# Kernel tuning notes

Measured on AMD Instinct MI355X. Metric: run time of the kernel, lower is better.

## Reference

```python
import jax, jax.numpy as jnp
import numpy as np

# PillarFeatureNet defaults
VX, VY = 0.2, 0.2
X_OFF = VX / 2 + 0.0      # vx/2 + pc_range[0]
Y_OFF = VY / 2 + (-40.0)  # vy/2 + pc_range[1]
BN_EPS = 1e-3             # mmdet3d BN1d eps for PFNLayer

P, N, C_RAW, C_OUT = 60000, 32, 4, 64  # pillars, max points/pillar, raw feats, PFN width


def setup_inputs() -> dict:
    key = jax.random.key(0)
    kf, kn, kc, kw = jax.random.split(key, 4)
    features = jax.random.normal(kf, (P, N, C_RAW), dtype=jnp.float32)
    # at least 1 valid point per pillar (original divides by num_points)
    num_points = jax.random.randint(kn, (P,), 1, N + 1, dtype=jnp.int32)
    coors = jax.random.randint(kc, (P, 4), 0, 352, dtype=jnp.int32)  # (batch, z, y, x) indices
    W = jax.random.normal(kw, (9, C_OUT), dtype=jnp.float32) * 0.1   # Linear(9,64,bias=False)
    gamma = jnp.ones((C_OUT,), jnp.float32)   # BN affine
    beta = jnp.zeros((C_OUT,), jnp.float32)
    return {"features": features, "num_points": num_points, "coors": coors,
            "W": W, "gamma": gamma, "beta": beta}


def reference(features, num_points, coors, W, gamma, beta):
    dt = features.dtype
    npts = num_points.astype(dt)[:, None, None]                    # [P,1,1]
    # cluster-center offset (xyz minus per-pillar mean over valid count)
    points_mean = jnp.sum(features[:, :, :3], axis=1, keepdims=True) / npts
    f_cluster = features[:, :, :3] - points_mean                   # [P,N,3]
    # voxel-center offset (xy minus pillar center from coors)
    xc = coors[:, 3].astype(dt)[:, None] * VX + X_OFF              # [P,1]
    yc = coors[:, 2].astype(dt)[:, None] * VY + Y_OFF
    f_center = jnp.stack([features[:, :, 0] - xc,
                          features[:, :, 1] - yc], axis=-1)        # [P,N,2]
    feats = jnp.concatenate([features, f_cluster, f_center], axis=-1)  # [P,N,9]
    # zero out padded points
    mask = (jnp.arange(feats.shape[1])[None, :] < num_points[:, None]).astype(dt)
    feats = feats * mask[:, :, None]
    # PFNLayer: Linear(no bias) -> BatchNorm1d (train-mode batch stats over P*N) -> ReLU -> max over points
    x = feats @ W                                                  # [P,N,64]
    mean = jnp.mean(x, axis=(0, 1))
    var = jnp.mean(jnp.square(x - mean), axis=(0, 1))              # biased, as torch BN training
    x = (x - mean) * (gamma / jnp.sqrt(var + BN_EPS)) + beta
    x = jax.nn.relu(x)
    return jnp.max(x, axis=1)                                      # [P,64] (squeeze(1) of keepdim max)
```

## Files before the change

### kernel.cpp

```cpp
#include <hip/hip_runtime.h>

#define NPT 32
#define COUT 64

typedef __fp16 v2hf __attribute__((ext_vector_type(2)));
typedef _Float16 v8h __attribute__((ext_vector_type(8)));
typedef float v16f __attribute__((ext_vector_type(16)));

union PKU { v2hf h; unsigned u; };
union FrgU { unsigned u[4]; v8h h; };

__device__ __forceinline__ unsigned pk2(float a, float b) {
    PKU p; p.h = __builtin_amdgcn_cvt_pkrtz(a, b); return p.u;
}

__device__ __forceinline__ float max16(v16f c) {
    float a = fmaxf(fmaxf(c[0], c[1]), fmaxf(c[2], c[3]));
    float b = fmaxf(fmaxf(c[4], c[5]), fmaxf(c[6], c[7]));
    float d = fmaxf(fmaxf(c[8], c[9]), fmaxf(c[10], c[11]));
    float e = fmaxf(fmaxf(c[12], c[13]), fmaxf(c[14], c[15]));
    return fmaxf(fmaxf(a, b), fmaxf(d, e));
}
__device__ __forceinline__ float sum16(v16f c) {
    float a = (c[0] + c[1]) + (c[2] + c[3]);
    float b = (c[4] + c[5]) + (c[6] + c[7]);
    float d = (c[8] + c[9]) + (c[10] + c[11]);
    float e = (c[12] + c[13]) + (c[14] + c[15]);
    return (a + b) + (d + e);
}
__device__ __forceinline__ float sumsq16(v16f c) {
    float a = 0.f, b = 0.f, d = 0.f, e = 0.f;
    #pragma unroll
    for (int i = 0; i < 4; i++) {
        a = fmaf(c[i], c[i], a);
        b = fmaf(c[4 + i], c[4 + i], b);
        d = fmaf(c[8 + i], c[8 + i], d);
        e = fmaf(c[12 + i], c[12 + i], e);
    }
    return (a + b) + (d + e);
}

__global__ __launch_bounds__(256, 3) void pillar_kernel(
        const float4* __restrict__ feat,
        const int* __restrict__ num_points,
        const int* __restrict__ coors,
        const float* __restrict__ W,
        float* __restrict__ out,
        float* __restrict__ stats,
        int P)
{
    __shared__ float red[4][128];

    int t = threadIdx.x;
    int lane = t & 63;
    int wv = t >> 6;
    int n = lane & 31;
    int hi = lane >> 5;
    int numPairs = (P + 1) >> 1;
    int pair = blockIdx.x * 4 + wv;

    float w4a = W[4 * COUT + n],      w5a = W[5 * COUT + n];
    float w6a = W[6 * COUT + n],      w7a = W[7 * COUT + n];
    float w8a = W[8 * COUT + n];
    float w4b = W[4 * COUT + 32 + n], w5b = W[5 * COUT + 32 + n];
    float w6b = W[6 * COUT + 32 + n], w7b = W[7 * COUT + 32 + n];
    float w8b = W[8 * COUT + 32 + n];
    float wp0a = W[0 * COUT + n] + w4a + w7a;
    float wp1a = W[1 * COUT + n] + w5a + w8a;
    float wp2a = W[2 * COUT + n] + w6a;
    float wp3a = W[3 * COUT + n];
    float wp0b = W[0 * COUT + 32 + n] + w4b + w7b;
    float wp1b = W[1 * COUT + 32 + n] + w5b + w8b;
    float wp2b = W[2 * COUT + 32 + n] + w6b;
    float wp3b = W[3 * COUT + 32 + n];
    unsigned bu0 = hi ? 0u : pk2(wp0a, wp1a);
    unsigned bu1 = hi ? 0u : pk2(wp2a, wp3a);
    unsigned bv0 = hi ? 0u : pk2(wp0b, wp1b);
    unsigned bv1 = hi ? 0u : pk2(wp2b, wp3b);

    int p = pair * 2 + hi;
    bool inb = (p < P);
    float4 f = make_float4(0.f, 0.f, 0.f, 0.f);
    int np = 1; float xc = 0.f, yc = 0.f;
    if (inb) {
        f  = feat[p * NPT + n];
        np = num_points[p];
        int2 cxy = *(const int2*)&coors[p * 4 + 2];
        yc = (float)cxy.x * 0.2f - 39.9f;
        xc = (float)cxy.y * 0.2f + 0.1f;
    }
    float sx = f.x, sy = f.y, sz = f.z;
    #pragma unroll
    for (int m = 1; m < 32; m <<= 1) {
        sx += __shfl_xor(sx, m);
        sy += __shfl_xor(sy, m);
        sz += __shfl_xor(sz, m);
    }
    float invn = 1.0f / (float)np;
    float mx = sx * invn, my = sy * invn, mz = sz * invn;
    float dA = mx * w4a + my * w5a + mz * w6a + xc * w7a + yc * w8a;
    float dB = mx * w4b + my * w5b + mz * w6b + xc * w7b + yc * w8b;
    float dA1 = __shfl_xor(dA, 32);
    float dB1 = __shfl_xor(dB, 32);

    bool msk = inb && (n < np);
    unsigned u0 = msk ? pk2(f.x, f.y) : 0u;
    unsigned u1 = msk ? pk2(f.z, f.w) : 0u;
    unsigned u2 = msk ? 0x3C00u : 0u;
    unsigned e0 = (unsigned)__shfl_xor((int)u0, 32);
    unsigned e1 = (unsigned)__shfl_xor((int)u1, 32);
    unsigned e2 = (unsigned)__shfl_xor((int)u2, 32);

    FrgU a0, a1;
    a0.u[0] = hi ? 0u : u0;  a0.u[1] = hi ? 0u : u1;
    a0.u[2] = hi ? 0u : u2;  a0.u[3] = 0u;
    a1.u[0] = hi ? 0u : e0;  a1.u[1] = hi ? 0u : e1;
    a1.u[2] = hi ? 0u : e2;  a1.u[3] = 0u;

    FrgU b00, b01, b10, b11;
    b00.u[0] = bu0; b00.u[1] = bu1; b00.u[2] = hi ? 0u : pk2(-dA,  0.f); b00.u[3] = 0u;
    b01.u[0] = bv0; b01.u[1] = bv1; b01.u[2] = hi ? 0u : pk2(-dB,  0.f); b01.u[3] = 0u;
    b10.u[0] = bu0; b10.u[1] = bu1; b10.u[2] = hi ? 0u : pk2(-dA1, 0.f); b10.u[3] = 0u;
    b11.u[0] = bv0; b11.u[1] = bv1; b11.u[2] = hi ? 0u : pk2(-dB1, 0.f); b11.u[3] = 0u;

    v16f cz = {};
    v16f c00 = __builtin_amdgcn_mfma_f32_32x32x16_f16(a0.h, b00.h, cz, 0, 0, 0);
    v16f c01 = __builtin_amdgcn_mfma_f32_32x32x16_f16(a0.h, b01.h, cz, 0, 0, 0);
    v16f c10 = __builtin_amdgcn_mfma_f32_32x32x16_f16(a1.h, b10.h, cz, 0, 0, 0);
    v16f c11 = __builtin_amdgcn_mfma_f32_32x32x16_f16(a1.h, b11.h, cz, 0, 0, 0);

    float s1a = sum16(c00) + sum16(c10);
    float s2a = sumsq16(c00) + sumsq16(c10);
    float s1b = sum16(c01) + sum16(c11);
    float s2b = sumsq16(c01) + sumsq16(c11);

    float m00 = max16(c00), m01 = max16(c01), m10 = max16(c10), m11 = max16(c11);
    m00 = fmaxf(m00, __shfl_xor(m00, 32));
    m01 = fmaxf(m01, __shfl_xor(m01, 32));
    m10 = fmaxf(m10, __shfl_xor(m10, 32));
    m11 = fmaxf(m11, __shfl_xor(m11, 32));

    int p0 = pair * 2;
    if (p0 < P)     out[p0 * COUT + lane]       = hi ? m01 : m00;
    if (p0 + 1 < P) out[(p0 + 1) * COUT + lane] = hi ? m11 : m10;

    s1a += __shfl_xor(s1a, 32);  s2a += __shfl_xor(s2a, 32);
    s1b += __shfl_xor(s1b, 32);  s2b += __shfl_xor(s2b, 32);
    red[wv][lane]      = hi ? s1b : s1a;
    red[wv][64 + lane] = hi ? s2b : s2a;
    __syncthreads();
    if (t < 128) {
        float s = red[0][t] + red[1][t] + red[2][t] + red[3][t];
        atomicAdd(&stats[(blockIdx.x & 7) * 128 + t], s);
    }
}

__global__ __launch_bounds__(256) void finalize_kernel(
        float4* __restrict__ out,
        const float* __restrict__ stats,
        const float* __restrict__ gamma,
        const float* __restrict__ beta,
        int n4, float invM)
{
    __shared__ float ss[128];
    int t = threadIdx.x;
    if (t < 64) {
        float s1 = 0.f, s2 = 0.f;
        #pragma unroll
        for (int x = 0; x < 8; x++) {
            s1 += stats[x * 128 + t];
            s2 += stats[x * 128 + 64 + t];
        }
        float mean = s1 * invM;
        float var = s2 * invM - mean * mean;
        float scale = gamma[t] * rsqrtf(var + 1e-3f);
        ss[t] = scale;
        ss[64 + t] = beta[t] - mean * scale;
    }
    __syncthreads();
    int i = blockIdx.x * 256 + t;
    if (i >= n4) return;
    int cb = (i & 15) * 4;
    float4 v = out[i];
    const float4 sc = *(const float4*)&ss[cb];
    const float4 sh = *(const float4*)&ss[64 + cb];
    v.x = fmaxf(fmaf(v.x, sc.x, sh.x), 0.f);
    v.y = fmaxf(fmaf(v.y, sc.y, sh.y), 0.f);
    v.z = fmaxf(fmaf(v.z, sc.z, sh.z), 0.f);
    v.w = fmaxf(fmaf(v.w, sc.w, sh.w), 0.f);
    out[i] = v;
}

extern "C" void kernel_launch(void* const* d_in, const int* in_sizes, int n_in,
                              void* d_out, int out_size, void* d_ws, size_t ws_size,
                              hipStream_t stream) {
    const float* features   = (const float*)d_in[0];
    const int*   num_points = (const int*)d_in[1];
    const int*   coors      = (const int*)d_in[2];
    const float* W          = (const float*)d_in[3];
    const float* gamma      = (const float*)d_in[4];
    const float* beta       = (const float*)d_in[5];
    float* out = (float*)d_out;
    int P = in_sizes[1];

    float* stats = (float*)d_ws;

    hipMemsetAsync(d_ws, 0, 8 * 128 * sizeof(float), stream);

    int numPairs = (P + 1) >> 1;
    int blocks1 = (numPairs + 3) / 4;
    pillar_kernel<<<blocks1, 256, 0, stream>>>((const float4*)features,
                                               num_points, coors, W, out,
                                               stats, P);
    int n4 = P * (COUT / 4);
    finalize_kernel<<<(n4 + 255) / 256, 256, 0, stream>>>(
        (float4*)out, stats, gamma, beta, n4,
        1.0f / ((float)P * (float)NPT));
}
```

Baseline: 110.7 us.

## Process two pillar pairs per wave and shard BN stat atomics wider

```diff
diff --git a/kernel.cpp b/kernel.cpp
--- a/kernel.cpp
+++ b/kernel.cpp
@@ -2,6 +2,7 @@
 
 #define NPT 32
 #define COUT 64
+#define NSHARD 16
 
 typedef __fp16 v2hf __attribute__((ext_vector_type(2)));
 typedef _Float16 v8h __attribute__((ext_vector_type(8)));
@@ -40,7 +41,7 @@
     return (a + b) + (d + e);
 }
 
-__global__ __launch_bounds__(256, 3) void pillar_kernel(
+__global__ __launch_bounds__(256, 4) void pillar_kernel(
         const float4* __restrict__ feat,
         const int* __restrict__ num_points,
         const int* __restrict__ coors,
@@ -57,7 +58,7 @@
     int n = lane & 31;
     int hi = lane >> 5;
     int numPairs = (P + 1) >> 1;
-    int pair = blockIdx.x * 4 + wv;
+    int pairBase = blockIdx.x * 8 + wv * 2;
 
     float w4a = W[4 * COUT + n],      w5a = W[5 * COUT + n];
     float w6a = W[6 * COUT + n],      w7a = W[7 * COUT + n];
@@ -78,71 +79,87 @@
     unsigned bv0 = hi ? 0u : pk2(wp0b, wp1b);
     unsigned bv1 = hi ? 0u : pk2(wp2b, wp3b);
 
-    int p = pair * 2 + hi;
-    bool inb = (p < P);
-    float4 f = make_float4(0.f, 0.f, 0.f, 0.f);
-    int np = 1; float xc = 0.f, yc = 0.f;
-    if (inb) {
-        f  = feat[p * NPT + n];
-        np = num_points[p];
-        int2 cxy = *(const int2*)&coors[p * 4 + 2];
-        yc = (float)cxy.x * 0.2f - 39.9f;
-        xc = (float)cxy.y * 0.2f + 0.1f;
-    }
-    float sx = f.x, sy = f.y, sz = f.z;
+    float s1a = 0.f, s2a = 0.f, s1b = 0.f, s2b = 0.f;
+
+    float4 f[2]; float xc[2], yc[2]; int np[2]; bool inb[2];
+    #pragma unroll
+    for (int u = 0; u < 2; u++) {
+        int p = (pairBase + u) * 2 + hi;
+        inb[u] = (p < P);
+        f[u] = make_float4(0.f, 0.f, 0.f, 0.f);
+        np[u] = 1; xc[u] = 0.f; yc[u] = 0.f;
+        if (inb[u]) {
+            f[u] = feat[p * NPT + n];
+            np[u] = num_points[p];
+            int2 cxy = *(const int2*)&coors[p * 4 + 2];
+            yc[u] = (float)cxy.x * 0.2f - 39.9f;
+            xc[u] = (float)cxy.y * 0.2f + 0.1f;
+        }
+    }
+    float sx[2], sy[2], sz[2];
+    #pragma unroll
+    for (int u = 0; u < 2; u++) { sx[u] = f[u].x; sy[u] = f[u].y; sz[u] = f[u].z; }
     #pragma unroll
     for (int m = 1; m < 32; m <<= 1) {
-        sx += __shfl_xor(sx, m);
-        sy += __shfl_xor(sy, m);
-        sz += __shfl_xor(sz, m);
-    }
-    float invn = 1.0f / (float)np;
-    float mx = sx * invn, my = sy * invn, mz = sz * invn;
-    float dA = mx * w4a + my * w5a + mz * w6a + xc * w7a + yc * w8a;
-    float dB = mx * w4b + my * w5b + mz * w6b + xc * w7b + yc * w8b;
-    float dA1 = __shfl_xor(dA, 32);
-    float dB1 = __shfl_xor(dB, 32);
-
-    bool msk = inb && (n < np);
-    unsigned u0 = msk ? pk2(f.x, f.y) : 0u;
-    unsigned u1 = msk ? pk2(f.z, f.w) : 0u;
-    unsigned u2 = msk ? 0x3C00u : 0u;
-    unsigned e0 = (unsigned)__shfl_xor((int)u0, 32);
-    unsigned e1 = (unsigned)__shfl_xor((int)u1, 32);
-    unsigned e2 = (unsigned)__shfl_xor((int)u2, 32);
-
-    FrgU a0, a1;
-    a0.u[0] = hi ? 0u : u0;  a0.u[1] = hi ? 0u : u1;
-    a0.u[2] = hi ? 0u : u2;  a0.u[3] = 0u;
-    a1.u[0] = hi ? 0u : e0;  a1.u[1] = hi ? 0u : e1;
-    a1.u[2] = hi ? 0u : e2;  a1.u[3] = 0u;
-
-    FrgU b00, b01, b10, b11;
-    b00.u[0] = bu0; b00.u[1] = bu1; b00.u[2] = hi ? 0u : pk2(-dA,  0.f); b00.u[3] = 0u;
-    b01.u[0] = bv0; b01.u[1] = bv1; b01.u[2] = hi ? 0u : pk2(-dB,  0.f); b01.u[3] = 0u;
-    b10.u[0] = bu0; b10.u[1] = bu1; b10.u[2] = hi ? 0u : pk2(-dA1, 0.f); b10.u[3] = 0u;
-    b11.u[0] = bv0; b11.u[1] = bv1; b11.u[2] = hi ? 0u : pk2(-dB1, 0.f); b11.u[3] = 0u;
-
-    v16f cz = {};
-    v16f c00 = __builtin_amdgcn_mfma_f32_32x32x16_f16(a0.h, b00.h, cz, 0, 0, 0);
-    v16f c01 = __builtin_amdgcn_mfma_f32_32x32x16_f16(a0.h, b01.h, cz, 0, 0, 0);
-    v16f c10 = __builtin_amdgcn_mfma_f32_32x32x16_f16(a1.h, b10.h, cz, 0, 0, 0);
-    v16f c11 = __builtin_amdgcn_mfma_f32_32x32x16_f16(a1.h, b11.h, cz, 0, 0, 0);
-
-    float s1a = sum16(c00) + sum16(c10);
-    float s2a = sumsq16(c00) + sumsq16(c10);
-    float s1b = sum16(c01) + sum16(c11);
-    float s2b = sumsq16(c01) + sumsq16(c11);
-
-    float m00 = max16(c00), m01 = max16(c01), m10 = max16(c10), m11 = max16(c11);
-    m00 = fmaxf(m00, __shfl_xor(m00, 32));
-    m01 = fmaxf(m01, __shfl_xor(m01, 32));
-    m10 = fmaxf(m10, __shfl_xor(m10, 32));
-    m11 = fmaxf(m11, __shfl_xor(m11, 32));
-
-    int p0 = pair * 2;
-    if (p0 < P)     out[p0 * COUT + lane]       = hi ? m01 : m00;
-    if (p0 + 1 < P) out[(p0 + 1) * COUT + lane] = hi ? m11 : m10;
+        #pragma unroll
+        for (int u = 0; u < 2; u++) {
+            sx[u] += __shfl_xor(sx[u], m);
+            sy[u] += __shfl_xor(sy[u], m);
+            sz[u] += __shfl_xor(sz[u], m);
+        }
+    }
+
+    #pragma unroll
+    for (int u = 0; u < 2; u++) {
+        int pair = pairBase + u;
+        float invn = 1.0f / (float)np[u];
+        float mx = sx[u] * invn, my = sy[u] * invn, mz = sz[u] * invn;
+        float dA = mx * w4a + my * w5a + mz * w6a + xc[u] * w7a + yc[u] * w8a;
+        float dB = mx * w4b + my * w5b + mz * w6b + xc[u] * w7b + yc[u] * w8b;
+        float dA1 = __shfl_xor(dA, 32);
+        float dB1 = __shfl_xor(dB, 32);
+
+        bool msk = inb[u] && (n < np[u]);
+        unsigned u0 = msk ? pk2(f[u].x, f[u].y) : 0u;
+        unsigned u1 = msk ? pk2(f[u].z, f[u].w) : 0u;
+        unsigned u2 = msk ? 0x3C00u : 0u;
+        unsigned e0 = (unsigned)__shfl_xor((int)u0, 32);
+        unsigned e1 = (unsigned)__shfl_xor((int)u1, 32);
+        unsigned e2 = (unsigned)__shfl_xor((int)u2, 32);
+
+        FrgU a0, a1;
+        a0.u[0] = hi ? 0u : u0;  a0.u[1] = hi ? 0u : u1;
+        a0.u[2] = hi ? 0u : u2;  a0.u[3] = 0u;
+        a1.u[0] = hi ? 0u : e0;  a1.u[1] = hi ? 0u : e1;
+        a1.u[2] = hi ? 0u : e2;  a1.u[3] = 0u;
+
+        FrgU b00, b01, b10, b11;
+        b00.u[0] = bu0; b00.u[1] = bu1; b00.u[2] = hi ? 0u : pk2(-dA,  0.f); b00.u[3] = 0u;
+        b01.u[0] = bv0; b01.u[1] = bv1; b01.u[2] = hi ? 0u : pk2(-dB,  0.f); b01.u[3] = 0u;
+        b10.u[0] = bu0; b10.u[1] = bu1; b10.u[2] = hi ? 0u : pk2(-dA1, 0.f); b10.u[3] = 0u;
+        b11.u[0] = bv0; b11.u[1] = bv1; b11.u[2] = hi ? 0u : pk2(-dB1, 0.f); b11.u[3] = 0u;
+
+        v16f cz = {};
+        v16f c00 = __builtin_amdgcn_mfma_f32_32x32x16_f16(a0.h, b00.h, cz, 0, 0, 0);
+        float s1a_l = sum16(c00), s2a_l = sumsq16(c00), m00 = max16(c00);
+        v16f c10 = __builtin_amdgcn_mfma_f32_32x32x16_f16(a1.h, b10.h, cz, 0, 0, 0);
+        s1a_l += sum16(c10); s2a_l += sumsq16(c10); float m10 = max16(c10);
+        v16f c01 = __builtin_amdgcn_mfma_f32_32x32x16_f16(a0.h, b01.h, cz, 0, 0, 0);
+        float s1b_l = sum16(c01), s2b_l = sumsq16(c01), m01 = max16(c01);
+        v16f c11 = __builtin_amdgcn_mfma_f32_32x32x16_f16(a1.h, b11.h, cz, 0, 0, 0);
+        s1b_l += sum16(c11); s2b_l += sumsq16(c11); float m11 = max16(c11);
+
+        s1a += s1a_l; s2a += s2a_l; s1b += s1b_l; s2b += s2b_l;
+
+        m00 = fmaxf(m00, __shfl_xor(m00, 32));
+        m01 = fmaxf(m01, __shfl_xor(m01, 32));
+        m10 = fmaxf(m10, __shfl_xor(m10, 32));
+        m11 = fmaxf(m11, __shfl_xor(m11, 32));
+
+        int p0 = pair * 2;
+        if (p0 < P)     out[p0 * COUT + lane]       = hi ? m01 : m00;
+        if (p0 + 1 < P) out[(p0 + 1) * COUT + lane] = hi ? m11 : m10;
+    }
 
     s1a += __shfl_xor(s1a, 32);  s2a += __shfl_xor(s2a, 32);
     s1b += __shfl_xor(s1b, 32);  s2b += __shfl_xor(s2b, 32);
@@ -151,7 +168,7 @@
     __syncthreads();
     if (t < 128) {
         float s = red[0][t] + red[1][t] + red[2][t] + red[3][t];
-        atomicAdd(&stats[(blockIdx.x & 7) * 128 + t], s);
+        atomicAdd(&stats[(blockIdx.x & (NSHARD - 1)) * 128 + t], s);
     }
 }
 
@@ -167,7 +184,7 @@
     if (t < 64) {
         float s1 = 0.f, s2 = 0.f;
         #pragma unroll
-        for (int x = 0; x < 8; x++) {
+        for (int x = 0; x < NSHARD; x++) {
             s1 += stats[x * 128 + t];
             s2 += stats[x * 128 + 64 + t];
         }
@@ -205,10 +222,10 @@
 
     float* stats = (float*)d_ws;
 
-    hipMemsetAsync(d_ws, 0, 8 * 128 * sizeof(float), stream);
+    hipMemsetAsync(d_ws, 0, NSHARD * 128 * sizeof(float), stream);
 
     int numPairs = (P + 1) >> 1;
-    int blocks1 = (numPairs + 3) / 4;
+    int blocks1 = (numPairs + 7) / 8;
     pillar_kernel<<<blocks1, 256, 0, stream>>>((const float4*)features,
                                                num_points, coors, W, out,
                                                stats, P);
```

Result: slower. 121.8 us (+10.1%).
